# Performance work log

Hardware: AMD Instinct MI355X
Metric: run time of the kernel (lower is better)

Reference implementation:

```python
import jax, jax.numpy as jnp
import numpy as np

Z, H, W = 8, 96, 192
WZ, WH, WW = 2, 6, 12
C, HEADS, DEPTH, B = 192, 6, 2, 1
NZ, NH, NW = Z // WZ, H // WH, W // WW
LW = WZ * WH * WW            # 144 tokens per window
WIN_TYPES = NZ * NH          # 64 earth-specific window types
NPOS = WZ * WZ * WH * WH * (2 * WW - 1)  # 3312 relative-position entries
HD = C // HEADS
SCALE = HD ** -0.5
SZ, SH, SW = WZ // 2, WH // 2, WW // 2


def _position_index():
    czi = np.arange(WZ); czj = -np.arange(WZ) * WZ
    chi = np.arange(WH); chj = -np.arange(WH) * WH
    cw = np.arange(WW)
    c1 = np.stack(np.meshgrid(czi, chi, cw, indexing='ij'), 0).reshape(3, -1)
    c2 = np.stack(np.meshgrid(czj, chj, cw, indexing='ij'), 0).reshape(3, -1)
    coords = (c1[:, :, None] - c2[:, None, :]).transpose(1, 2, 0).astype(np.int64).copy()
    coords[:, :, 2] += WW - 1
    coords[:, :, 1] *= 2 * WW - 1
    coords[:, :, 0] *= (2 * WW - 1) * WH * WH
    return coords.sum(-1).reshape(-1)


def _attention_mask():
    m = np.zeros((Z, H, W))
    zs = (slice(0, -WZ), slice(-WZ, -SZ), slice(-SZ, None))
    hs = (slice(0, -WH), slice(-WH, -SH), slice(-SH, None))
    ws = (slice(0, -WW), slice(-WW, -SW), slice(-SW, None))
    cnt = 0
    for z in zs:
        for h in hs:
            for w in ws:
                m[z, h, w] = cnt
                cnt += 1
    mw = m.reshape(NZ, WZ, NH, WH, NW, WW).transpose(0, 2, 4, 1, 3, 5).reshape(-1, LW)
    d = mw[:, None, :] - mw[:, :, None]
    return np.where(d != 0, -100.0, 0.0).astype(np.float32)


def setup_inputs() -> dict:
    key = jax.random.key(0)
    ks = jax.random.split(key, 12)
    s = 0.02
    def rn(k, shape):
        return jax.random.normal(k, shape, jnp.float32) * s
    return {
        'x': jax.random.normal(ks[0], (B, Z * H * W, C), jnp.float32),
        'qkv_w': rn(ks[1], (DEPTH, C, 3 * C)),
        'qkv_b': rn(ks[2], (DEPTH, 3 * C)),
        'proj_w': rn(ks[3], (DEPTH, C, C)),
        'proj_b': rn(ks[4], (DEPTH, C)),
        'bias_tab': rn(ks[5], (DEPTH, NPOS, WIN_TYPES, HEADS)),
        'n1_g': jnp.ones((DEPTH, C), jnp.float32),
        'n1_b': jnp.zeros((DEPTH, C), jnp.float32),
        'n2_g': jnp.ones((DEPTH, C), jnp.float32),
        'n2_b': jnp.zeros((DEPTH, C), jnp.float32),
        'mlp_w1': rn(ks[6], (DEPTH, C, 4 * C)),
        'mlp_b1': rn(ks[7], (DEPTH, 4 * C)),
        'mlp_w2': rn(ks[8], (DEPTH, 4 * C, C)),
        'mlp_b2': rn(ks[9], (DEPTH, C)),
        'pos_index': jnp.asarray(_position_index(), jnp.int32),
        'attn_mask': jnp.asarray(_attention_mask()),
    }


def _ln(x, g, b):
    m = x.mean(-1, keepdims=True)
    v = jnp.mean((x - m) ** 2, -1, keepdims=True)
    return (x - m) / jnp.sqrt(v + 1e-5) * g + b


def _forward(x, qkv_w, qkv_b, proj_w, proj_b, bias_tab, n1_g, n1_b, n2_g, n2_b,
             mlp_w1, mlp_b1, mlp_w2, mlp_b2, pos_index, attn_mask):
    for blk in range(DEPTH):
        roll = (blk % 2 == 1)
        shortcut = x
        h = _ln(x, n1_g[blk], n1_b[blk]).reshape(B, Z, H, W, C)
        if roll:
            h = jnp.roll(h, (-SZ, -SH, -SW), (1, 2, 3))
        # partition windows: (B*nZ*nH*nW, LW, C)
        h = h.reshape(B, NZ, WZ, NH, WH, NW, WW, C).transpose(0, 1, 3, 5, 2, 4, 6, 7).reshape(-1, LW, C)
        B_ = h.shape[0]
        qkv = (h @ qkv_w[blk] + qkv_b[blk]).reshape(B_, LW, 3, HEADS, HD)
        q = qkv[:, :, 0].transpose(0, 2, 1, 3) * SCALE  # (B_, heads, LW, hd)
        k = qkv[:, :, 1].transpose(0, 2, 1, 3)
        v = qkv[:, :, 2].transpose(0, 2, 1, 3)
        attn = jnp.einsum('bhid,bhjd->bhij', q, k)
        # earth-specific bias gathered by relative-position index
        bias = bias_tab[blk][pos_index].reshape(LW, LW, WIN_TYPES, HEADS).transpose(2, 3, 0, 1)
        attn = (attn.reshape(-1, WIN_TYPES, HEADS, LW, LW) + bias).reshape(B_, HEADS, LW, LW)
        if roll:
            attn = (attn.reshape(B, WIN_TYPES * NW, HEADS, LW, LW) + attn_mask[None, :, None]).reshape(B_, HEADS, LW, LW)
        attn = jax.nn.softmax(attn, -1)
        o = jnp.einsum('bhij,bhjd->bhid', attn, v).transpose(0, 2, 1, 3).reshape(B_, LW, C)
        o = o @ proj_w[blk] + proj_b[blk]
        # reverse windows
        o = o.reshape(B, NZ, NH, NW, WZ, WH, WW, C).transpose(0, 1, 4, 2, 5, 3, 6, 7).reshape(B, Z, H, W, C)
        if roll:
            o = jnp.roll(o, (SZ, SH, SW), (1, 2, 3))
        x = shortcut + o.reshape(B, Z * H * W, C)
        h2 = _ln(x, n2_g[blk], n2_b[blk])
        h2 = jax.nn.gelu(h2 @ mlp_w1[blk] + mlp_b1[blk], approximate=False) @ mlp_w2[blk] + mlp_b2[blk]
        x = x + h2
    return x


def reference(x, qkv_w, qkv_b, proj_w, proj_b, bias_tab, n1_g, n1_b, n2_g, n2_b,
              mlp_w1, mlp_b1, mlp_w2, mlp_b2, pos_index, attn_mask):
    return _forward(x, qkv_w, qkv_b, proj_w, proj_b, bias_tab, n1_g, n1_b, n2_g, n2_b,
                    mlp_w1, mlp_b1, mlp_w2, mlp_b2, pos_index, attn_mask)
```

## Files before the change

### kernel.cpp

```cpp
#include <hip/hip_runtime.h>
#include <math.h>

#define TZ 8
#define TH 96
#define TW 192
#define C 192
#define NHEADS 6
#define HDIM 32
#define LW 144
#define NWIN 1024
#define NTOK 147456
#define NPOS 3312
#define QSCALE 0.17677669529663687f

typedef unsigned short u16;
typedef __attribute__((ext_vector_type(8))) short bf8_t;
typedef __attribute__((ext_vector_type(4))) short bf4_t;
typedef __attribute__((ext_vector_type(4))) unsigned short us4_t;
typedef __attribute__((ext_vector_type(4))) float f4_t;

__device__ __forceinline__ float bf2f(u16 u) {
    union { unsigned int i; float f; } c; c.i = ((unsigned int)u) << 16; return c.f;
}
__device__ __forceinline__ u16 f2bf(float f) {
    union { float f; unsigned int i; } c; c.f = f;
    unsigned int x = c.i;
    x += 0x7fffu + ((x >> 16) & 1u);
    return (u16)(x >> 16);
}

__device__ __forceinline__ int win_row_to_token(int r, int roll) {
    int wi = r / LW, l = r % LW;
    int nz = wi >> 8, nh = (wi >> 4) & 15, nw = wi & 15;
    int iz = l / 72, rr = l % 72, ih = rr / 12, iw = rr % 12;
    int z = nz * 2 + iz, h = nh * 6 + ih, w = nw * 12 + iw;
    if (roll) {
        z = (z + 1) & 7;
        h += 3; if (h >= TH) h -= TH;
        w += 6; if (w >= TW) w -= TW;
    }
    return (z * TH + h) * TW + w;
}

__global__ __launch_bounds__(256) void ln_kernel(
    const float* __restrict__ x, const float* __restrict__ g,
    const float* __restrict__ b, u16* __restrict__ xnc,
    int windowed, int roll)
{
    int wave = threadIdx.x >> 6;
    int lane = threadIdx.x & 63;
    int d = blockIdx.x * 4 + wave;
    int src = windowed ? win_row_to_token(d, roll) : d;
    const float* xr = x + (size_t)src * C;
    float v0 = xr[lane], v1 = xr[lane + 64], v2 = xr[lane + 128];
    float s = v0 + v1 + v2;
    float sq = v0 * v0 + v1 * v1 + v2 * v2;
    #pragma unroll
    for (int off = 32; off > 0; off >>= 1) {
        s  += __shfl_xor(s, off, 64);
        sq += __shfl_xor(sq, off, 64);
    }
    float mean = s * (1.0f / 192.0f);
    float var  = sq * (1.0f / 192.0f) - mean * mean;
    float rstd = rsqrtf(var + 1e-5f);
    u16* orow = xnc + (size_t)d * C;
    orow[lane]       = f2bf((v0 - mean) * rstd * g[lane]       + b[lane]);
    orow[lane + 64]  = f2bf((v1 - mean) * rstd * g[lane + 64]  + b[lane + 64]);
    orow[lane + 128] = f2bf((v2 - mean) * rstd * g[lane + 128] + b[lane + 128]);
}

__global__ __launch_bounds__(256) void tconv_kernel(
    const float* __restrict__ W, u16* __restrict__ WT, int K, int N)
{
    int idx = blockIdx.x * 256 + threadIdx.x;
    if (idx >= N * K) return;
    int n = idx / K, k = idx % K;
    WT[idx] = f2bf(W[(size_t)k * N + n]);
}

__global__ __launch_bounds__(256) void biasmat_kernel(
    const float* __restrict__ btab, const int* __restrict__ pidx,
    u16* __restrict__ biasf)
{
    int wt = blockIdx.x, head = blockIdx.y;
    size_t obase = ((size_t)wt * 6 + head) * (LW * LW);
    for (int idx = threadIdx.x; idx < LW * LW; idx += 256) {
        int p = pidx[idx];
        biasf[obase + idx] = f2bf(btab[((size_t)p * 64 + wt) * 6 + head]);
    }
}

template <int MODE>
__global__ __launch_bounds__(256) void mm_kernel(
    const u16* __restrict__ A, const u16* __restrict__ BT,
    const float* __restrict__ bias, void* __restrict__ Cvoid,
    int N, int K, int roll)
{
    __shared__ alignas(16) u16 As[128 * 72];
    __shared__ alignas(16) u16 Bs[64 * 72];
    int tid = threadIdx.x;
    int mb = blockIdx.y * 128, nb = blockIdx.x * 64;
    int wave = tid >> 6, lane = tid & 63;
    int mh = wave >> 1, nh = wave & 1;
    int lr = lane & 15, g = lane >> 4;

    f4_t acc[4][2];
    #pragma unroll
    for (int mi = 0; mi < 4; mi++)
        #pragma unroll
        for (int ni = 0; ni < 2; ni++)
            acc[mi][ni] = (f4_t){0.f, 0.f, 0.f, 0.f};

    for (int k0 = 0; k0 < K; k0 += 64) {
        #pragma unroll
        for (int it = 0; it < 4; it++) {
            int idx = it * 256 + tid;
            int r = idx >> 3, kc = idx & 7;
            *(bf8_t*)&As[r * 72 + kc * 8] =
                *(const bf8_t*)&A[(size_t)(mb + r) * K + k0 + kc * 8];
        }
        #pragma unroll
        for (int it = 0; it < 2; it++) {
            int idx = it * 256 + tid;
            int r = idx >> 3, kc = idx & 7;
            *(bf8_t*)&Bs[r * 72 + kc * 8] =
                *(const bf8_t*)&BT[(size_t)(nb + r) * K + k0 + kc * 8];
        }
        __syncthreads();
        #pragma unroll
        for (int ks = 0; ks < 2; ks++) {
            bf8_t bfr[2];
            #pragma unroll
            for (int ni = 0; ni < 2; ni++)
                bfr[ni] = *(const bf8_t*)&Bs[(nh * 32 + ni * 16 + lr) * 72 + ks * 32 + g * 8];
            #pragma unroll
            for (int mi = 0; mi < 4; mi++) {
                bf8_t afr = *(const bf8_t*)&As[(mh * 64 + mi * 16 + lr) * 72 + ks * 32 + g * 8];
                #pragma unroll
                for (int ni = 0; ni < 2; ni++)
                    acc[mi][ni] = __builtin_amdgcn_mfma_f32_16x16x32_bf16(
                        afr, bfr[ni], acc[mi][ni], 0, 0, 0);
            }
        }
        __syncthreads();
    }

    #pragma unroll
    for (int mi = 0; mi < 4; mi++) {
        int rbase = mb + mh * 64 + mi * 16 + g * 4;
        int tok[4];
        if (MODE == 1) {
            #pragma unroll
            for (int r = 0; r < 4; r++)
                tok[r] = win_row_to_token(rbase + r, roll);
        }
        #pragma unroll
        for (int ni = 0; ni < 2; ni++) {
            int col = nb + nh * 32 + ni * 16 + lr;
            float bb = bias[col];
            #pragma unroll
            for (int r = 0; r < 4; r++) {
                float v = acc[mi][ni][r] + bb;
                if (MODE == 0) {
                    if (col < 192) v *= QSCALE;
                    ((u16*)Cvoid)[(size_t)(rbase + r) * 576 + col] = f2bf(v);
                } else if (MODE == 1) {
                    ((float*)Cvoid)[(size_t)tok[r] * C + col] += v;
                } else if (MODE == 2) {
                    v = 0.5f * v * (1.0f + erff(v * 0.70710678118654752f));
                    ((u16*)Cvoid)[(size_t)(rbase + r) * 768 + col] = f2bf(v);
                } else {
                    ((float*)Cvoid)[(size_t)(rbase + r) * C + col] += v;
                }
            }
        }
    }
}

template <int ROLL>
__global__ __launch_bounds__(192, 4) void attn_kernel(
    const u16* __restrict__ qkvb, const u16* __restrict__ biasf,
    u16* __restrict__ attnb)
{
    __shared__ alignas(16) u16 Qs[144 * 40];
    __shared__ alignas(16) u16 Ks[144 * 40];
    __shared__ alignas(16) u16 Vt[32 * 148];
    __shared__ unsigned char region8[148];

    int bid = blockIdx.x;
    int xcd = bid & 7, slot = bid >> 3;
    int p   = xcd * 48 + (slot >> 4);
    int rep = slot & 15;
    int wt = p / 6, head = p - wt * 6;
    int nh = (rep & 3) * 4 + (wt >> 4);
    int wl = (rep >> 2) * 256 + nh * 16 + (wt & 15);
    int tid = threadIdx.x;

    const u16* base = qkvb + (size_t)wl * LW * 576;
    for (int c = tid; c < 576; c += 192) {
        int l = c >> 2, d8 = (c & 3) << 3;
        const u16* row = base + (size_t)l * 576 + head * 32;
        *(bf8_t*)&Qs[l * 40 + d8] = *(const bf8_t*)&row[d8];
        *(bf8_t*)&Ks[l * 40 + d8] = *(const bf8_t*)&row[192 + d8];
        bf8_t v8 = *(const bf8_t*)&row[384 + d8];
        #pragma unroll
        for (int m = 0; m < 8; m++)
            Vt[(d8 + m) * 148 + l] = (u16)v8[m];
    }
    bool doMask = false;
    if (ROLL) {
        int nz = wl >> 8, nw = wl & 15;
        doMask = (nz == 3) || (nh == 15) || (nw == 15);
        if (tid < 144) {
            int iz = tid / 72, rr = tid % 72, ih = rr / 12, iw = rr % 12;
            int z = nz * 2 + iz, h = nh * 6 + ih, w = nw * 12 + iw;
            int rz = (z < 6) ? 0 : ((z < 7) ? 1 : 2);
            int rh = (h < 90) ? 0 : ((h < 93) ? 1 : 2);
            int rw2 = (w < 180) ? 0 : ((w < 186) ? 1 : 2);
            region8[tid] = (unsigned char)(rz * 9 + rh * 3 + rw2);
        }
    }
    __syncthreads();

    int wave = tid >> 6, lane = tid & 63;
    int lr = lane & 15, g = lane >> 4;
    int jb = g << 2;
    const f4_t z4 = {0.f, 0.f, 0.f, 0.f};

    for (int itl = 0; itl < 3; itl++) {
        int it = wave * 3 + itl;
        int i_row = it * 16 + lr;
        bf8_t qf = *(const bf8_t*)&Qs[i_row * 40 + (g << 3)];
        f4_t s[9];
        #pragma unroll
        for (int jt = 0; jt < 9; jt++) {
            bf8_t kf = *(const bf8_t*)&Ks[(jt * 16 + lr) * 40 + (g << 3)];
            s[jt] = __builtin_amdgcn_mfma_f32_16x16x32_bf16(kf, qf, z4, 0, 0, 0);
        }

        const u16* bb = biasf + ((size_t)(wt * 6 + head) * LW + i_row) * LW;
        float m4[4] = {-1e30f, -1e30f, -1e30f, -1e30f};
        if (ROLL && doMask) {
            unsigned int ri = region8[i_row];
            #pragma unroll
            for (int jt = 0; jt < 9; jt++) {
                us4_t b4 = *(const us4_t*)&bb[jt * 16 + jb];
                unsigned int rj = *(const unsigned int*)&region8[jt * 16 + jb];
                #pragma unroll
                for (int r = 0; r < 4; r++) {
                    float v = s[jt][r] + bf2f(b4[r]);
                    if (((rj >> (8 * r)) & 255u) != ri) v -= 100.0f;
                    s[jt][r] = v;
                    m4[r] = fmaxf(m4[r], v);
                }
            }
        } else {
            #pragma unroll
            for (int jt = 0; jt < 9; jt++) {
                us4_t b4 = *(const us4_t*)&bb[jt * 16 + jb];
                #pragma unroll
                for (int r = 0; r < 4; r++) {
                    float v = s[jt][r] + bf2f(b4[r]);
                    s[jt][r] = v;
                    m4[r] = fmaxf(m4[r], v);
                }
            }
        }
        float m = fmaxf(fmaxf(m4[0], m4[1]), fmaxf(m4[2], m4[3]));
        m = fmaxf(m, __shfl_xor(m, 16, 64));
        m = fmaxf(m, __shfl_xor(m, 32, 64));

        float l4[4] = {0.f, 0.f, 0.f, 0.f};
        #pragma unroll
        for (int jt = 0; jt < 9; jt++)
            #pragma unroll
            for (int r = 0; r < 4; r++) {
                float pv = __expf(s[jt][r] - m);
                s[jt][r] = pv;
                l4[r] += pv;
            }
        float lsum = (l4[0] + l4[1]) + (l4[2] + l4[3]);
        lsum += __shfl_xor(lsum, 16, 64);
        lsum += __shfl_xor(lsum, 32, 64);
        float inv = 1.0f / lsum;

        bf8_t pfrag[5];
        #pragma unroll
        for (int t = 0; t < 4; t++)
            #pragma unroll
            for (int m2 = 0; m2 < 4; m2++) {
                pfrag[t][m2]     = (short)f2bf(s[2 * t][m2] * inv);
                pfrag[t][4 + m2] = (short)f2bf(s[2 * t + 1][m2] * inv);
            }
        #pragma unroll
        for (int m2 = 0; m2 < 4; m2++) {
            pfrag[4][m2]     = (short)f2bf(s[8][m2] * inv);
            pfrag[4][4 + m2] = 0;
        }

        #pragma unroll
        for (int dt = 0; dt < 2; dt++) {
            const u16* vrow = &Vt[(dt * 16 + lr) * 148];
            f4_t acc = z4;
            #pragma unroll
            for (int t = 0; t < 5; t++) {
                bf4_t va = *(const bf4_t*)&vrow[t * 32 + jb];
                bf8_t af;
                #pragma unroll
                for (int m2 = 0; m2 < 4; m2++) af[m2] = va[m2];
                if (t < 4) {
                    bf4_t vb = *(const bf4_t*)&vrow[t * 32 + 16 + jb];
                    #pragma unroll
                    for (int m2 = 0; m2 < 4; m2++) af[4 + m2] = vb[m2];
                } else {
                    #pragma unroll
                    for (int m2 = 0; m2 < 4; m2++) af[4 + m2] = 0;
                }
                acc = __builtin_amdgcn_mfma_f32_16x16x32_bf16(af, pfrag[t], acc, 0, 0, 0);
            }
            us4_t o;
            #pragma unroll
            for (int r = 0; r < 4; r++) o[r] = f2bf(acc[r]);
            *(us4_t*)&attnb[((size_t)wl * LW + i_row) * 192 + head * 32 + dt * 16 + jb] = o;
        }
    }
}

extern "C" void kernel_launch(void* const* d_in, const int* in_sizes, int n_in,
                              void* d_out, int out_size, void* d_ws, size_t ws_size,
                              hipStream_t stream)
{
    (void)in_sizes; (void)n_in; (void)out_size; (void)ws_size;
    const float* x_in   = (const float*)d_in[0];
    const float* qkv_w  = (const float*)d_in[1];
    const float* qkv_b  = (const float*)d_in[2];
    const float* proj_w = (const float*)d_in[3];
    const float* proj_b = (const float*)d_in[4];
    const float* btab   = (const float*)d_in[5];
    const float* n1g    = (const float*)d_in[6];
    const float* n1b    = (const float*)d_in[7];
    const float* n2g    = (const float*)d_in[8];
    const float* n2b    = (const float*)d_in[9];
    const float* w1     = (const float*)d_in[10];
    const float* b1     = (const float*)d_in[11];
    const float* w2     = (const float*)d_in[12];
    const float* b2     = (const float*)d_in[13];
    const int*   pidx   = (const int*)d_in[14];

    float* x   = (float*)d_out;
    u16* biasf = (u16*)d_ws;
    u16* wT    = biasf + (size_t)64 * 6 * LW * LW;
    u16* xnc   = wT + 884736;
    u16* qkvb  = xnc + (size_t)NTOK * C;
    u16* attnb = qkvb + (size_t)NTOK * 576;
    u16* hidb  = qkvb;

    const size_t WBLK = 442368;
    const size_t OQKV = 0, OPROJ = 110592, OW1 = 147456, OW2 = 294912;

    hipMemcpyAsync(x, x_in, (size_t)NTOK * C * sizeof(float),
                   hipMemcpyDeviceToDevice, stream);

    for (int blk = 0; blk < 2; blk++) {
        u16* wb = wT + blk * WBLK;
        tconv_kernel<<<(576 * 192 + 255) / 256, 256, 0, stream>>>(
            qkv_w + (size_t)blk * C * 576, wb + OQKV, C, 576);
        tconv_kernel<<<(192 * 192 + 255) / 256, 256, 0, stream>>>(
            proj_w + (size_t)blk * C * C, wb + OPROJ, C, 192);
        tconv_kernel<<<(768 * 192 + 255) / 256, 256, 0, stream>>>(
            w1 + (size_t)blk * C * 768, wb + OW1, C, 768);
        tconv_kernel<<<(192 * 768 + 255) / 256, 256, 0, stream>>>(
            w2 + (size_t)blk * 768 * C, wb + OW2, 768, 192);
    }

    for (int blk = 0; blk < 2; blk++) {
        int roll = blk & 1;
        u16* wb = wT + blk * WBLK;
        biasmat_kernel<<<dim3(64, 6), 256, 0, stream>>>(
            btab + (size_t)blk * NPOS * 64 * 6, pidx, biasf);
        ln_kernel<<<NTOK / 4, 256, 0, stream>>>(
            x, n1g + blk * C, n1b + blk * C, xnc, 1, roll);
        mm_kernel<0><<<dim3(9, NTOK / 128), 256, 0, stream>>>(
            xnc, wb + OQKV, qkv_b + blk * 576, qkvb, 576, C, roll);
        if (roll)
            attn_kernel<1><<<NWIN * NHEADS, 192, 0, stream>>>(qkvb, biasf, attnb);
        else
            attn_kernel<0><<<NWIN * NHEADS, 192, 0, stream>>>(qkvb, biasf, attnb);
        mm_kernel<1><<<dim3(3, NTOK / 128), 256, 0, stream>>>(
            attnb, wb + OPROJ, proj_b + blk * C, x, 192, C, roll);
        ln_kernel<<<NTOK / 4, 256, 0, stream>>>(
            x, n2g + blk * C, n2b + blk * C, xnc, 0, 0);
        mm_kernel<2><<<dim3(12, NTOK / 128), 256, 0, stream>>>(
            xnc, wb + OW1, b1 + blk * 768, hidb, 768, C, 0);
        mm_kernel<3><<<dim3(3, NTOK / 128), 256, 0, stream>>>(
            hidb, wb + OW2, b2 + blk * C, x, 192, 768, 0);
    }
}
```

Before: 1.659 ms.

## Store QKV and attention output in head-major 32-wide planes

The QKV GEMM now writes its output as separate head-major planes of 32 columns per token, so each attention block reads contiguous Q, K and V slabs instead of strided 576-wide rows. The attention output uses the same plane layout, and the projection GEMM's A-load indexes into it. The XCD-aware block remapping in the attention kernel is replaced by a plain 2D grid of windows by heads, which gives up the bias-matrix locality that remapping was meant to provide. GEMM epilogue stores become more scattered across planes.

```diff
diff --git a/kernel.cpp b/kernel.cpp
--- a/kernel.cpp
+++ b/kernel.cpp
@@ -116,8 +116,13 @@
         for (int it = 0; it < 4; it++) {
             int idx = it * 256 + tid;
             int r = idx >> 3, kc = idx & 7;
-            *(bf8_t*)&As[r * 72 + kc * 8] =
-                *(const bf8_t*)&A[(size_t)(mb + r) * K + k0 + kc * 8];
+            int kk = k0 + kc * 8;
+            const u16* srcp;
+            if (MODE == 1)
+                srcp = &A[((size_t)(kk >> 5) * NTOK + (mb + r)) * 32 + (kk & 31)];
+            else
+                srcp = &A[(size_t)(mb + r) * K + kk];
+            *(bf8_t*)&As[r * 72 + kc * 8] = *(const bf8_t*)srcp;
         }
         #pragma unroll
         for (int it = 0; it < 2; it++) {
@@ -163,7 +168,8 @@
                 float v = acc[mi][ni][r] + bb;
                 if (MODE == 0) {
                     if (col < 192) v *= QSCALE;
-                    ((u16*)Cvoid)[(size_t)(rbase + r) * 576 + col] = f2bf(v);
+                    ((u16*)Cvoid)[((size_t)(col >> 5) * NTOK + (rbase + r)) * 32 + (col & 31)]
+                        = f2bf(v);
                 } else if (MODE == 1) {
                     ((float*)Cvoid)[(size_t)tok[r] * C + col] += v;
                 } else if (MODE == 2) {
@@ -187,33 +193,29 @@
     __shared__ alignas(16) u16 Vt[32 * 148];
     __shared__ unsigned char region8[148];
 
-    int bid = blockIdx.x;
-    int xcd = bid & 7, slot = bid >> 3;
-    int p   = xcd * 48 + (slot >> 4);
-    int rep = slot & 15;
-    int wt = p / 6, head = p - wt * 6;
-    int nh = (rep & 3) * 4 + (wt >> 4);
-    int wl = (rep >> 2) * 256 + nh * 16 + (wt & 15);
+    int wl = blockIdx.x, head = blockIdx.y;
+    int wt = wl & 63;
     int tid = threadIdx.x;
 
-    const u16* base = qkvb + (size_t)wl * LW * 576;
+    const u16* qp = qkvb + ((size_t)(0 * 6 + head) * NTOK + (size_t)wl * LW) * 32;
+    const u16* kp = qkvb + ((size_t)(1 * 6 + head) * NTOK + (size_t)wl * LW) * 32;
+    const u16* vp = qkvb + ((size_t)(2 * 6 + head) * NTOK + (size_t)wl * LW) * 32;
     for (int c = tid; c < 576; c += 192) {
         int l = c >> 2, d8 = (c & 3) << 3;
-        const u16* row = base + (size_t)l * 576 + head * 32;
-        *(bf8_t*)&Qs[l * 40 + d8] = *(const bf8_t*)&row[d8];
-        *(bf8_t*)&Ks[l * 40 + d8] = *(const bf8_t*)&row[192 + d8];
-        bf8_t v8 = *(const bf8_t*)&row[384 + d8];
+        *(bf8_t*)&Qs[l * 40 + d8] = *(const bf8_t*)&qp[l * 32 + d8];
+        *(bf8_t*)&Ks[l * 40 + d8] = *(const bf8_t*)&kp[l * 32 + d8];
+        bf8_t v8 = *(const bf8_t*)&vp[l * 32 + d8];
         #pragma unroll
         for (int m = 0; m < 8; m++)
             Vt[(d8 + m) * 148 + l] = (u16)v8[m];
     }
     bool doMask = false;
     if (ROLL) {
-        int nz = wl >> 8, nw = wl & 15;
-        doMask = (nz == 3) || (nh == 15) || (nw == 15);
+        int nz = wl >> 8, nhh = (wl >> 4) & 15, nw = wl & 15;
+        doMask = (nz == 3) || (nhh == 15) || (nw == 15);
         if (tid < 144) {
             int iz = tid / 72, rr = tid % 72, ih = rr / 12, iw = rr % 12;
-            int z = nz * 2 + iz, h = nh * 6 + ih, w = nw * 12 + iw;
+            int z = nz * 2 + iz, h = nhh * 6 + ih, w = nw * 12 + iw;
             int rz = (z < 6) ? 0 : ((z < 7) ? 1 : 2);
             int rh = (h < 90) ? 0 : ((h < 93) ? 1 : 2);
             int rw2 = (w < 180) ? 0 : ((w < 186) ? 1 : 2);
@@ -226,6 +228,7 @@
     int lr = lane & 15, g = lane >> 4;
     int jb = g << 2;
     const f4_t z4 = {0.f, 0.f, 0.f, 0.f};
+    u16* op = attnb + ((size_t)head * NTOK + (size_t)wl * LW) * 32;
 
     for (int itl = 0; itl < 3; itl++) {
         int it = wave * 3 + itl;
@@ -321,7 +324,7 @@
             us4_t o;
             #pragma unroll
             for (int r = 0; r < 4; r++) o[r] = f2bf(acc[r]);
-            *(us4_t*)&attnb[((size_t)wl * LW + i_row) * 192 + head * 32 + dt * 16 + jb] = o;
+            *(us4_t*)&op[(size_t)i_row * 32 + dt * 16 + jb] = o;
         }
     }
 }
@@ -383,9 +386,9 @@
         mm_kernel<0><<<dim3(9, NTOK / 128), 256, 0, stream>>>(
             xnc, wb + OQKV, qkv_b + blk * 576, qkvb, 576, C, roll);
         if (roll)
-            attn_kernel<1><<<NWIN * NHEADS, 192, 0, stream>>>(qkvb, biasf, attnb);
+            attn_kernel<1><<<dim3(NWIN, NHEADS), 192, 0, stream>>>(qkvb, biasf, attnb);
         else
-            attn_kernel<0><<<NWIN * NHEADS, 192, 0, stream>>>(qkvb, biasf, attnb);
+            attn_kernel<0><<<dim3(NWIN, NHEADS), 192, 0, stream>>>(qkvb, biasf, attnb);
         mm_kernel<1><<<dim3(3, NTOK / 128), 256, 0, stream>>>(
             attnb, wb + OPROJ, proj_b + blk * C, x, 192, C, roll);
         ln_kernel<<<NTOK / 4, 256, 0, stream>>>(
```

New measurement: 1.645 ms. No clear change (-0.8%).
